# Kernel tuning notes

Hardware: AMD Instinct MI355X
Metric: run time of the kernel (lower is better)

Reference implementation:

```python
import jax, jax.numpy as jnp
import numpy as np

N_EMBED = 512  # codebook size per Quantize
EPS = 1e-8


def _quantize(x, embed):
    # x: (L, d) flattened tokens; embed: (d, K) codebook
    # squared euclidean distance via expansion (as in torch source)
    dist = (x * x).sum(1, keepdims=True) - 2.0 * (x @ embed) + (embed * embed).sum(0, keepdims=True)
    ind = jnp.argmin(dist, axis=1)                      # (L,)
    q = jnp.take(embed.T, ind, axis=0)                  # (L, d) embedding lookup
    diff = jnp.mean((jax.lax.stop_gradient(q) - x) ** 2)
    q_st = x + jax.lax.stop_gradient(q - x)             # straight-through
    return q_st, diff, ind


def _ot_score(x, embed):
    # x: (L, d); embed: (d, K). OT score = sum_k (1 - cos_sim) * softmax(x@embed / K)
    xn = x / (jnp.linalg.norm(x, axis=1, keepdims=True) + EPS)
    en = embed / (jnp.linalg.norm(embed, axis=0, keepdims=True) + EPS)
    cos_dissim = jax.lax.stop_gradient(1.0 - xn @ en)   # torch version uses .data (no grad)
    cnd = jax.nn.softmax((x @ embed) * (1.0 / embed.shape[1]), axis=1)
    return (cos_dissim * cnd).sum(1)                    # (L,)


def setup_inputs() -> dict:
    key = jax.random.key(0)
    k1, k2, k3, k4 = jax.random.split(key, 4)
    n_levels, B, L, d = 5, 128, 196, 64
    input_list = jax.random.normal(k1, (n_levels, B, L, d), dtype=jnp.float32)
    cb_top = jax.random.normal(k2, (15, d, N_EMBED), dtype=jnp.float32)        # quantize_list_5
    cb_lvl = jax.random.normal(k3, (4, 15, 2 * d, N_EMBED), dtype=jnp.float32)  # quantize_list_1..4
    label = jax.random.randint(k4, (B,), 0, 15, dtype=jnp.int32)
    return {"input_list": input_list, "cb_top": cb_top, "cb_lvl": cb_lvl, "label": label}


def reference(input_list, cb_top, cb_lvl, label):
    # Hierarchical switch-VQ encode (eval mode): top level quantized with per-class
    # codebook, then each lower level concatenated with top quantized code and
    # quantized with its own per-class codebook; last level also computes OT score.
    vq = jax.vmap(_quantize)
    emb_top = cb_top[label]                              # (B, 64, 512) per-sample codebook
    q4, d4, _ = vq(input_list[4], emb_top)               # (B, L, 64)
    diff = d4.sum()
    quants, ids = [], []
    ot_score = None
    for j in (3, 2, 1, 0):                               # quantize_list_4, _3, _2, _1
        x = jnp.concatenate([input_list[j], q4], axis=-1)  # (B, L, 128)
        emb = cb_lvl[j][label]                           # (B, 128, 512)
        q, d, i = vq(x, emb)
        diff = diff + d.sum()
        quants.append(q)
        ids.append(i)
        if j == 0:                                       # OT=True level
            ot_score = jax.vmap(_ot_score)(x, emb)       # (B, L)
    quant_list = jnp.stack(quants)                       # (4, B, L, 128)
    id_list = jnp.stack(ids)                             # (4, B, L)
    return quant_list, diff, id_list, ot_score
```

## Files before the change

### kernel.cpp

```cpp
#include <hip/hip_runtime.h>
#include <hip/hip_bf16.h>
#include <math.h>

#define B 128
#define L 196
#define K 512
#define NCLS 15
#define NT 32
#define NTILES 7

#define DIFF_OFF 12845056
#define ID_OFF   12845057
#define OT_OFF   12945409

#define WS_Q4   0
#define WS_N2   1605632
#define WS_INVE 1644032
#define WS_CBT  1651712
#define CBT_LVL 491520
#define WS_EBT_BYTES ((size_t)(1651712 + 4423680) * 4)
#define EBT_LVL_BYTES 983040

#define BAND 2.5f
#define CCAP 384

typedef __attribute__((ext_vector_type(8))) short s16x8;
typedef __attribute__((ext_vector_type(4))) float f32x4;
typedef __attribute__((ext_vector_type(4))) unsigned short u16x4;

__device__ inline unsigned short f2bf(float f) {
    __hip_bfloat16 h = __float2bfloat16(f);
    return *reinterpret_cast<unsigned short*>(&h);
}

__global__ __launch_bounds__(256) void precompute(
    const float* __restrict__ cb_top, const float* __restrict__ cb_lvl,
    float* __restrict__ ws)
{
    __shared__ float Ld[128][65];
    __shared__ float ps[64][4];
    const int m = blockIdx.x >> 3;
    const int c0 = (blockIdx.x & 7) * 64;
    const bool top = m < NCLS;
    const int D = top ? 64 : 128;
    const float* src = top ? cb_top + (size_t)m * 64 * K
                           : cb_lvl + (size_t)(m - NCLS) * 128 * K;
    float* cbT = ws + WS_CBT + (top ? (size_t)m * K * 64
                                    : (size_t)CBT_LVL + (size_t)(m - NCLS) * K * 128);
    unsigned short* ebt = (unsigned short*)((char*)ws + WS_EBT_BYTES +
        (top ? (size_t)m * K * 64 * 2
             : (size_t)EBT_LVL_BYTES + (size_t)(m - NCLS) * K * 128 * 2));
    const int tid = threadIdx.x;

    for (int e = tid; e < D * 64; e += 256) {
        int d = e >> 6, cc = e & 63;
        Ld[d][cc] = src[(size_t)d * K + c0 + cc];
    }
    __syncthreads();

    const int col = tid >> 2, q = tid & 3;
    const int seg = D >> 2;
    float ss = 0.f;
    for (int i = 0; i < seg; ++i) {
        int d = q * seg + i;
        float v = Ld[d][col];
        ss = fmaf(v, v, ss);
        cbT[(size_t)(c0 + col) * D + d] = v;
        ebt[(size_t)(c0 + col) * D + d] = f2bf(v);
    }
    ps[col][q] = ss;
    __syncthreads();
    if (tid < 64) {
        float n2 = (ps[tid][0] + ps[tid][1]) + (ps[tid][2] + ps[tid][3]);
        ws[WS_N2 + (size_t)m * K + c0 + tid] = n2;
        if (m >= NCLS && m < 2 * NCLS)
            ws[WS_INVE + (size_t)(m - NCLS) * K + c0 + tid] = 1.f / (sqrtf(n2) + 1e-8f);
    }
}

template<int D, bool IS_TOP, bool OT>
__global__ __launch_bounds__(256, 4) void vq_fused(
    const float* __restrict__ input, const int* __restrict__ label,
    float* __restrict__ ws, float* __restrict__ out, int jbase)
{
    constexpr int XS = D + 8;
    constexpr int NKS = D / 32;
    __shared__ unsigned short x_s[NT * XS];
    __shared__ float n2s[K];
    __shared__ float ivec[K];
    __shared__ float xn_s[NT];
    __shared__ float wmin_s[4][NT];
    __shared__ float rowMinG[NT];
    __shared__ unsigned int clist[CCAP];
    __shared__ float clv[CCAP];
    __shared__ int ccnt;
    __shared__ unsigned long long best_s[NT];
    __shared__ float otZ[4][NT], otW[4][NT];
    __shared__ float dred[4];

    const int tid = threadIdx.x;
    const int t0 = blockIdx.x * NT;
    const int b = blockIdx.y;
    const int j = IS_TOP ? 4 : (OT ? 0 : (int)blockIdx.z + jbase);
    const int c = label[b];

    const float* xin = input + ((size_t)((IS_TOP ? 4 : j) * B + b) * L) * 64;
    const float* q4w = ws + WS_Q4 + (size_t)b * L * 64;
    const float* n2w = ws + WS_N2 + (size_t)(IS_TOP ? c : NCLS + j * NCLS + c) * K;
    const char*  ebt = (const char*)ws + WS_EBT_BYTES +
        (IS_TOP ? (size_t)c * K * 64 * 2
                : (size_t)EBT_LVL_BYTES + (size_t)(j * NCLS + c) * K * 128 * 2);
    const float* cbT = ws + WS_CBT +
        (IS_TOP ? (size_t)c * K * 64
                : (size_t)CBT_LVL + (size_t)(j * NCLS + c) * K * 128);

    if (tid < NT) { xn_s[tid] = 0.f; best_s[tid] = ~0ULL; }
    if (tid == 0) ccnt = 0;
    for (int i = tid; i < K; i += 256) {
        n2s[i] = n2w[i];
        if (OT) ivec[i] = ws[WS_INVE + (size_t)c * K + i];
    }
    __syncthreads();

    for (int idx = tid; idx < NT * D / 4; idx += 256) {
        int row = idx / (D / 4);
        int k4 = (idx % (D / 4)) * 4;
        int l = t0 + row;
        float4 v = make_float4(0.f, 0.f, 0.f, 0.f);
        if (l < L) {
            const float* p = (IS_TOP || k4 < 64) ? xin + (size_t)l * 64 + k4
                                                 : q4w + (size_t)l * 64 + (k4 - 64);
            v = *reinterpret_cast<const float4*>(p);
            atomicAdd(&xn_s[row], v.x * v.x + v.y * v.y + v.z * v.z + v.w * v.w);
        }
        u16x4 h;
        h[0] = f2bf(v.x); h[1] = f2bf(v.y); h[2] = f2bf(v.z); h[3] = f2bf(v.w);
        *reinterpret_cast<u16x4*>(&x_s[row * XS + k4]) = h;
    }
    __syncthreads();

    const int wid = tid >> 6, lane = tid & 63;
    const int l15 = lane & 15, l4 = lane >> 4;

    float runMin[2][4];
    float zS[2][4], wS[2][4];
    #pragma unroll
    for (int mi = 0; mi < 2; ++mi)
        #pragma unroll
        for (int r = 0; r < 4; ++r) {
            runMin[mi][r] = 3.4e38f;
            if (OT) { zS[mi][r] = 0.f; wS[mi][r] = 0.f; }
        }

    for (int cc = 0; cc < 2; ++cc) {
        const int colbase = cc * 256 + wid * 64;
        f32x4 acc[2][4] = {};
        #pragma unroll
        for (int ks = 0; ks < NKS; ++ks) {
            s16x8 av[2], bv[4];
            #pragma unroll
            for (int mi = 0; mi < 2; ++mi)
                av[mi] = *reinterpret_cast<const s16x8*>(
                    &x_s[(mi * 16 + l15) * XS + ks * 32 + l4 * 8]);
            #pragma unroll
            for (int ni = 0; ni < 4; ++ni)
                bv[ni] = *reinterpret_cast<const s16x8*>(
                    ebt + ((size_t)(colbase + ni * 16 + l15) * D + ks * 32 + l4 * 8) * 2);
            #pragma unroll
            for (int mi = 0; mi < 2; ++mi)
                #pragma unroll
                for (int ni = 0; ni < 4; ++ni)
                    acc[mi][ni] = __builtin_amdgcn_mfma_f32_16x16x32_bf16(
                        av[mi], bv[ni], acc[mi][ni], 0, 0, 0);
        }
        #pragma unroll
        for (int mi = 0; mi < 2; ++mi) {
            #pragma unroll
            for (int r = 0; r < 4; ++r) {
                const int row = mi * 16 + l4 * 4 + r;
                const int lg = t0 + row;
                float dv[4];
                #pragma unroll
                for (int ni = 0; ni < 4; ++ni)
                    dv[ni] = n2s[colbase + ni * 16 + l15] - 2.f * acc[mi][ni][r];
                float mnW = fminf(fminf(dv[0], dv[1]), fminf(dv[2], dv[3]));
                #pragma unroll
                for (int s = 1; s <= 8; s <<= 1)
                    mnW = fminf(mnW, __shfl_xor(mnW, s, 64));
                runMin[mi][r] = fminf(runMin[mi][r], mnW);
                const float thr = runMin[mi][r] + BAND;
                if (lg < L) {
                    #pragma unroll
                    for (int ni = 0; ni < 4; ++ni) {
                        if (dv[ni] <= thr) {
                            int pos = atomicAdd(&ccnt, 1);
                            if (pos < CCAP) {
                                clist[pos] = ((unsigned)row << 16) |
                                             (unsigned)(colbase + ni * 16 + l15);
                                clv[pos] = dv[ni];
                            }
                        }
                    }
                }
                if (OT) {
                    float ivx = 1.f / (sqrtf(xn_s[row]) + 1e-8f);
                    #pragma unroll
                    for (int ni = 0; ni < 4; ++ni) {
                        float s = acc[mi][ni][r];
                        float e = __expf(s * (1.f / 512.f));
                        zS[mi][r] += e;
                        wS[mi][r] += (1.f - s * ivx * ivec[colbase + ni * 16 + l15]) * e;
                    }
                }
            }
        }
    }

    #pragma unroll
    for (int mi = 0; mi < 2; ++mi)
        #pragma unroll
        for (int r = 0; r < 4; ++r) {
            const int row = mi * 16 + l4 * 4 + r;
            if (l15 == 0) wmin_s[wid][row] = runMin[mi][r];
            if (OT) {
                float z = zS[mi][r], w = wS[mi][r];
                #pragma unroll
                for (int s = 1; s <= 8; s <<= 1) {
                    z += __shfl_xor(z, s, 64);
                    w += __shfl_xor(w, s, 64);
                }
                if (l15 == 0) { otZ[wid][row] = z; otW[wid][row] = w; }
            }
        }
    __syncthreads();
    if (tid < NT)
        rowMinG[tid] = fminf(fminf(wmin_s[0][tid], wmin_s[1][tid]),
                             fminf(wmin_s[2][tid], wmin_s[3][tid]));
    __syncthreads();

    {
        const int ncand = min(ccnt, CCAP);
        for (int e = wid; e < ncand; e += 4) {
            unsigned ent = clist[e];
            int row = ent >> 16, col = ent & 0xFFFF;
            if (clv[e] > rowMinG[row] + BAND) continue;
            int l = t0 + row;
            float prod;
            if (IS_TOP) {
                prod = xin[(size_t)l * 64 + lane] * cbT[(size_t)col * 64 + lane];
            } else {
                int k = lane * 2;
                const float* xp = (k < 64) ? &xin[(size_t)l * 64 + k]
                                           : &q4w[(size_t)l * 64 + (k - 64)];
                float2 xv = *reinterpret_cast<const float2*>(xp);
                float2 ev = *reinterpret_cast<const float2*>(&cbT[(size_t)col * 128 + k]);
                prod = xv.x * ev.x + xv.y * ev.y;
            }
            #pragma unroll
            for (int s = 1; s <= 32; s <<= 1) prod += __shfl_xor(prod, s, 64);
            if (lane == 0) {
                float dvE = n2s[col] - 2.f * prod;
                unsigned u = __float_as_uint(dvE);
                u = (u & 0x80000000u) ? ~u : (u | 0x80000000u);
                atomicMin(&best_s[row], ((unsigned long long)u << 32) | (unsigned)col);
            }
        }
    }
    __syncthreads();

    float dacc = 0.f;
    const int slot = IS_TOP ? 0 : 3 - j;
    for (int rr = wid; rr < NT; rr += 4) {
        int l = t0 + rr;
        if (l >= L) continue;
        unsigned long long key = best_s[rr];
        unsigned col = (unsigned)(key & 0xFFFFFFFFull);
        unsigned u = (unsigned)(key >> 32);
        u = (u & 0x80000000u) ? (u & 0x7FFFFFFFu) : ~u;
        float dvE = __uint_as_float(u);
        if (lane == 0) dacc += dvE + xn_s[rr];
        if (IS_TOP) {
            ws[WS_Q4 + ((size_t)b * L + l) * 64 + lane] = cbT[(size_t)col * 64 + lane];
        } else {
            int k = lane * 2;
            float2 ev = *reinterpret_cast<const float2*>(&cbT[(size_t)col * 128 + k]);
            *reinterpret_cast<float2*>(
                &out[(((size_t)slot * B + b) * L + l) * 128 + k]) = ev;
            if (lane == 0) {
                out[ID_OFF + ((size_t)slot * B + b) * L + l] = (float)col;
                if (OT) {
                    float z = (otZ[0][rr] + otZ[1][rr]) + (otZ[2][rr] + otZ[3][rr]);
                    float w = (otW[0][rr] + otW[1][rr]) + (otW[2][rr] + otW[3][rr]);
                    out[OT_OFF + (size_t)b * L + l] = w / z;
                }
            }
        }
    }
    if (lane == 0) dred[wid] = dacc;
    __syncthreads();
    if (tid == 0)
        atomicAdd(out + DIFF_OFF,
                  ((dred[0] + dred[1]) + (dred[2] + dred[3])) * (1.f / (L * (float)D)));
}

extern "C" void kernel_launch(void* const* d_in, const int* in_sizes, int n_in,
                              void* d_out, int out_size, void* d_ws, size_t ws_size,
                              hipStream_t stream) {
    const float* input  = (const float*)d_in[0];
    const float* cb_top = (const float*)d_in[1];
    const float* cb_lvl = (const float*)d_in[2];
    const int*   label  = (const int*)d_in[3];
    float* out = (float*)d_out;
    float* ws  = (float*)d_ws;

    hipMemsetAsync(out + DIFF_OFF, 0, sizeof(float), stream);

    precompute<<<600, 256, 0, stream>>>(cb_top, cb_lvl, ws);
    vq_fused<64, true, false><<<dim3(NTILES, B, 1), 256, 0, stream>>>(input, label, ws, out, 0);
    vq_fused<128, false, false><<<dim3(NTILES, B, 3), 256, 0, stream>>>(input, label, ws, out, 1);
    vq_fused<128, false, true><<<dim3(NTILES, B, 1), 256, 0, stream>>>(input, label, ws, out, 0);
}
```

Measured before the change: 327.0 us.

## Fuse top-level and lower-level VQ into one kernel, recomputing top per block

Replaces the three VQ launches (top level, then three lower levels, then the OT level) with one kernel over four levels. Each block recomputes the top-level quantization for its tile in shared memory instead of reading q4 from a global workspace written by a separate launch. This removes the launch serialization and the q4 round trip through global memory, at the cost of doing the top-level GEMM and refine four times. It also re-maps the refine and output phases to 16-lane groups with float4 loads, keeps n2 and inverse norms in registers, raises the candidate cap, and asks for occupancy 6.

```diff
diff --git a/kernel.cpp b/kernel.cpp
--- a/kernel.cpp
+++ b/kernel.cpp
@@ -13,16 +13,15 @@
 #define ID_OFF   12845057
 #define OT_OFF   12945409
 
-#define WS_Q4   0
-#define WS_N2   1605632
-#define WS_INVE 1644032
-#define WS_CBT  1651712
+#define WS_N2   0
+#define WS_INVE 38400
+#define WS_CBT  46080
 #define CBT_LVL 491520
-#define WS_EBT_BYTES ((size_t)(1651712 + 4423680) * 4)
+#define WS_EBT_BYTES ((size_t)(46080 + 4469760) * 4)
 #define EBT_LVL_BYTES 983040
 
 #define BAND 2.5f
-#define CCAP 384
+#define CCAP 512
 
 typedef __attribute__((ext_vector_type(8))) short s16x8;
 typedef __attribute__((ext_vector_type(4))) float f32x4;
@@ -78,94 +77,89 @@
     }
 }
 
-template<int D, bool IS_TOP, bool OT>
-__global__ __launch_bounds__(256, 4) void vq_fused(
+__global__ __launch_bounds__(256, 6) void vq_all(
     const float* __restrict__ input, const int* __restrict__ label,
-    float* __restrict__ ws, float* __restrict__ out, int jbase)
+    float* __restrict__ ws, float* __restrict__ out)
 {
-    constexpr int XS = D + 8;
-    constexpr int NKS = D / 32;
-    __shared__ unsigned short x_s[NT * XS];
-    __shared__ float n2s[K];
-    __shared__ float ivec[K];
-    __shared__ float xn_s[NT];
+    __shared__ char uA[8192];
+    __shared__ unsigned short xL_s[NT * 136];
+    __shared__ float clv[CCAP];
+    __shared__ unsigned int clist[CCAP];
     __shared__ float wmin_s[4][NT];
     __shared__ float rowMinG[NT];
-    __shared__ unsigned int clist[CCAP];
-    __shared__ float clv[CCAP];
+    __shared__ unsigned long long best_s[NT];
+    __shared__ float xn4_s[NT], xnL_s[NT], xnq_s[NT];
+    __shared__ float otZ_s[NT], otW_s[NT];
+    __shared__ float dacc_s;
     __shared__ int ccnt;
-    __shared__ unsigned long long best_s[NT];
-    __shared__ float otZ[4][NT], otW[4][NT];
-    __shared__ float dred[4];
+
+    unsigned short* x4_s = (unsigned short*)uA;
+    float* q4f = (float*)uA;
 
     const int tid = threadIdx.x;
     const int t0 = blockIdx.x * NT;
     const int b = blockIdx.y;
-    const int j = IS_TOP ? 4 : (OT ? 0 : (int)blockIdx.z + jbase);
+    const int j = blockIdx.z;
+    const bool OT = (j == 0);
+    const bool addTop = (j == 3);
     const int c = label[b];
 
-    const float* xin = input + ((size_t)((IS_TOP ? 4 : j) * B + b) * L) * 64;
-    const float* q4w = ws + WS_Q4 + (size_t)b * L * 64;
-    const float* n2w = ws + WS_N2 + (size_t)(IS_TOP ? c : NCLS + j * NCLS + c) * K;
-    const char*  ebt = (const char*)ws + WS_EBT_BYTES +
-        (IS_TOP ? (size_t)c * K * 64 * 2
-                : (size_t)EBT_LVL_BYTES + (size_t)(j * NCLS + c) * K * 128 * 2);
-    const float* cbT = ws + WS_CBT +
-        (IS_TOP ? (size_t)c * K * 64
-                : (size_t)CBT_LVL + (size_t)(j * NCLS + c) * K * 128);
-
-    if (tid < NT) { xn_s[tid] = 0.f; best_s[tid] = ~0ULL; }
-    if (tid == 0) ccnt = 0;
-    for (int i = tid; i < K; i += 256) {
-        n2s[i] = n2w[i];
-        if (OT) ivec[i] = ws[WS_INVE + (size_t)c * K + i];
-    }
-    __syncthreads();
-
-    for (int idx = tid; idx < NT * D / 4; idx += 256) {
-        int row = idx / (D / 4);
-        int k4 = (idx % (D / 4)) * 4;
+    const float* xin4 = input + ((size_t)(4 * B + b) * L) * 64;
+    const float* xinj = input + ((size_t)(j * B + b) * L) * 64;
+    const float* n2T = ws + WS_N2 + (size_t)c * K;
+    const float* n2L = ws + WS_N2 + (size_t)(NCLS + j * NCLS + c) * K;
+    const float* ive = ws + WS_INVE + (size_t)c * K;
+    const float* cbT_T = ws + WS_CBT + (size_t)c * (K * 64);
+    const float* cbT_L = ws + WS_CBT + CBT_LVL + (size_t)(j * NCLS + c) * (K * 128);
+    const unsigned short* ebT =
+        (const unsigned short*)((const char*)ws + WS_EBT_BYTES) + (size_t)c * (K * 64);
+    const unsigned short* ebL =
+        (const unsigned short*)((const char*)ws + WS_EBT_BYTES + EBT_LVL_BYTES) +
+        (size_t)(j * NCLS + c) * (K * 128);
+
+    const int wid = tid >> 6, lane = tid & 63, l15 = lane & 15, l4 = lane >> 4;
+
+    if (tid < NT) {
+        xn4_s[tid] = 0.f; xnL_s[tid] = 0.f; best_s[tid] = ~0ULL;
+        otZ_s[tid] = 0.f; otW_s[tid] = 0.f;
+    }
+    if (tid == 0) { ccnt = 0; dacc_s = 0.f; }
+    __syncthreads();
+
+    for (int idx = tid; idx < NT * 16; idx += 256) {
+        int row = idx >> 4, k4 = (idx & 15) << 2;
         int l = t0 + row;
         float4 v = make_float4(0.f, 0.f, 0.f, 0.f);
         if (l < L) {
-            const float* p = (IS_TOP || k4 < 64) ? xin + (size_t)l * 64 + k4
-                                                 : q4w + (size_t)l * 64 + (k4 - 64);
-            v = *reinterpret_cast<const float4*>(p);
-            atomicAdd(&xn_s[row], v.x * v.x + v.y * v.y + v.z * v.z + v.w * v.w);
-        }
-        u16x4 h;
-        h[0] = f2bf(v.x); h[1] = f2bf(v.y); h[2] = f2bf(v.z); h[3] = f2bf(v.w);
-        *reinterpret_cast<u16x4*>(&x_s[row * XS + k4]) = h;
-    }
-    __syncthreads();
-
-    const int wid = tid >> 6, lane = tid & 63;
-    const int l15 = lane & 15, l4 = lane >> 4;
+            v = *(const float4*)(xin4 + (size_t)l * 64 + k4);
+            atomicAdd(&xn4_s[row], v.x * v.x + v.y * v.y + v.z * v.z + v.w * v.w);
+        }
+        u16x4 h; h[0] = f2bf(v.x); h[1] = f2bf(v.y); h[2] = f2bf(v.z); h[3] = f2bf(v.w);
+        *(u16x4*)&x4_s[row * 72 + k4] = h;
+    }
+    __syncthreads();
 
     float runMin[2][4];
-    float zS[2][4], wS[2][4];
     #pragma unroll
     for (int mi = 0; mi < 2; ++mi)
         #pragma unroll
-        for (int r = 0; r < 4; ++r) {
-            runMin[mi][r] = 3.4e38f;
-            if (OT) { zS[mi][r] = 0.f; wS[mi][r] = 0.f; }
-        }
+        for (int r = 0; r < 4; ++r) runMin[mi][r] = 3.4e38f;
 
     for (int cc = 0; cc < 2; ++cc) {
         const int colbase = cc * 256 + wid * 64;
+        float n2v[4];
+        #pragma unroll
+        for (int ni = 0; ni < 4; ++ni) n2v[ni] = n2T[colbase + ni * 16 + l15];
         f32x4 acc[2][4] = {};
         #pragma unroll
-        for (int ks = 0; ks < NKS; ++ks) {
+        for (int ks = 0; ks < 2; ++ks) {
             s16x8 av[2], bv[4];
             #pragma unroll
             for (int mi = 0; mi < 2; ++mi)
-                av[mi] = *reinterpret_cast<const s16x8*>(
-                    &x_s[(mi * 16 + l15) * XS + ks * 32 + l4 * 8]);
+                av[mi] = *(const s16x8*)&x4_s[(mi * 16 + l15) * 72 + ks * 32 + l4 * 8];
             #pragma unroll
             for (int ni = 0; ni < 4; ++ni)
-                bv[ni] = *reinterpret_cast<const s16x8*>(
-                    ebt + ((size_t)(colbase + ni * 16 + l15) * D + ks * 32 + l4 * 8) * 2);
+                bv[ni] = *(const s16x8*)&ebT[(size_t)(colbase + ni * 16 + l15) * 64 + ks * 32 + l4 * 8];
             #pragma unroll
             for (int mi = 0; mi < 2; ++mi)
                 #pragma unroll
@@ -178,18 +172,156 @@
             #pragma unroll
             for (int r = 0; r < 4; ++r) {
                 const int row = mi * 16 + l4 * 4 + r;
-                const int lg = t0 + row;
                 float dv[4];
                 #pragma unroll
                 for (int ni = 0; ni < 4; ++ni)
-                    dv[ni] = n2s[colbase + ni * 16 + l15] - 2.f * acc[mi][ni][r];
+                    dv[ni] = n2v[ni] - 2.f * acc[mi][ni][r];
                 float mnW = fminf(fminf(dv[0], dv[1]), fminf(dv[2], dv[3]));
                 #pragma unroll
                 for (int s = 1; s <= 8; s <<= 1)
                     mnW = fminf(mnW, __shfl_xor(mnW, s, 64));
                 runMin[mi][r] = fminf(runMin[mi][r], mnW);
                 const float thr = runMin[mi][r] + BAND;
-                if (lg < L) {
+                if (t0 + row < L) {
+                    #pragma unroll
+                    for (int ni = 0; ni < 4; ++ni) {
+                        if (dv[ni] <= thr) {
+                            int pos = atomicAdd(&ccnt, 1);
+                            if (pos < CCAP) {
+                                clist[pos] = ((unsigned)row << 16) |
+                                             (unsigned)(colbase + ni * 16 + l15);
+                                clv[pos] = dv[ni];
+                            }
+                        }
+                    }
+                }
+            }
+        }
+    }
+    #pragma unroll
+    for (int mi = 0; mi < 2; ++mi)
+        #pragma unroll
+        for (int r = 0; r < 4; ++r)
+            if (l15 == 0) wmin_s[wid][mi * 16 + l4 * 4 + r] = runMin[mi][r];
+    __syncthreads();
+    if (tid < NT)
+        rowMinG[tid] = fminf(fminf(wmin_s[0][tid], wmin_s[1][tid]),
+                             fminf(wmin_s[2][tid], wmin_s[3][tid]));
+    __syncthreads();
+
+    {
+        const int ncand = min(ccnt, CCAP);
+        const int g = tid >> 4, li = tid & 15;
+        for (int e = g; e < ncand; e += 16) {
+            unsigned ent = clist[e];
+            int row = ent >> 16, col = ent & 0xFFFF;
+            if (clv[e] > rowMinG[row] + BAND) continue;
+            int l = t0 + row;
+            float4 xv = *(const float4*)(xin4 + (size_t)l * 64 + li * 4);
+            float4 ev = *(const float4*)(cbT_T + (size_t)col * 64 + li * 4);
+            float prod = xv.x * ev.x + xv.y * ev.y + xv.z * ev.z + xv.w * ev.w;
+            #pragma unroll
+            for (int s = 1; s <= 8; s <<= 1) prod += __shfl_xor(prod, s, 64);
+            if (li == 0) {
+                float dvE = n2T[col] - 2.f * prod;
+                unsigned u = __float_as_uint(dvE);
+                u = (u & 0x80000000u) ? ~u : (u | 0x80000000u);
+                atomicMin(&best_s[row], ((unsigned long long)u << 32) | (unsigned)col);
+            }
+        }
+    }
+    __syncthreads();
+
+    {
+        const int g = tid >> 4, li = tid & 15;
+        for (int rr = g; rr < NT; rr += 16) {
+            int l = t0 + rr;
+            unsigned long long key = best_s[rr];
+            float4 ev = make_float4(0.f, 0.f, 0.f, 0.f);
+            float dvE = 0.f;
+            if (l < L) {
+                unsigned col = (unsigned)(key & 0xFFFFFFFFull);
+                unsigned u = (unsigned)(key >> 32);
+                u = (u & 0x80000000u) ? (u & 0x7FFFFFFFu) : ~u;
+                dvE = __uint_as_float(u);
+                ev = *(const float4*)(cbT_T + (size_t)col * 64 + li * 4);
+            }
+            *(float4*)&q4f[rr * 64 + li * 4] = ev;
+            u16x4 h; h[0] = f2bf(ev.x); h[1] = f2bf(ev.y); h[2] = f2bf(ev.z); h[3] = f2bf(ev.w);
+            *(u16x4*)&xL_s[rr * 136 + 64 + li * 4] = h;
+            float qs = ev.x * ev.x + ev.y * ev.y + ev.z * ev.z + ev.w * ev.w;
+            #pragma unroll
+            for (int s = 1; s <= 8; s <<= 1) qs += __shfl_xor(qs, s, 64);
+            if (li == 0) {
+                xnq_s[rr] = qs;
+                if (addTop && l < L)
+                    atomicAdd(&dacc_s, (dvE + xn4_s[rr]) * (1.f / (L * 64.f)));
+            }
+        }
+    }
+    __syncthreads();
+
+    if (tid < NT) best_s[tid] = ~0ULL;
+    if (tid == 0) ccnt = 0;
+    for (int idx = tid; idx < NT * 16; idx += 256) {
+        int row = idx >> 4, k4 = (idx & 15) << 2;
+        int l = t0 + row;
+        float4 v = make_float4(0.f, 0.f, 0.f, 0.f);
+        if (l < L) {
+            v = *(const float4*)(xinj + (size_t)l * 64 + k4);
+            atomicAdd(&xnL_s[row], v.x * v.x + v.y * v.y + v.z * v.z + v.w * v.w);
+        }
+        u16x4 h; h[0] = f2bf(v.x); h[1] = f2bf(v.y); h[2] = f2bf(v.z); h[3] = f2bf(v.w);
+        *(u16x4*)&xL_s[row * 136 + k4] = h;
+    }
+    __syncthreads();
+
+    #pragma unroll
+    for (int mi = 0; mi < 2; ++mi)
+        #pragma unroll
+        for (int r = 0; r < 4; ++r) runMin[mi][r] = 3.4e38f;
+
+    for (int cc = 0; cc < 2; ++cc) {
+        const int colbase = cc * 256 + wid * 64;
+        float n2v[4], iv[4];
+        #pragma unroll
+        for (int ni = 0; ni < 4; ++ni) {
+            n2v[ni] = n2L[colbase + ni * 16 + l15];
+            if (OT) iv[ni] = ive[colbase + ni * 16 + l15];
+        }
+        f32x4 acc[2][4] = {};
+        #pragma unroll
+        for (int ks = 0; ks < 4; ++ks) {
+            s16x8 av[2], bv[4];
+            #pragma unroll
+            for (int mi = 0; mi < 2; ++mi)
+                av[mi] = *(const s16x8*)&xL_s[(mi * 16 + l15) * 136 + ks * 32 + l4 * 8];
+            #pragma unroll
+            for (int ni = 0; ni < 4; ++ni)
+                bv[ni] = *(const s16x8*)&ebL[(size_t)(colbase + ni * 16 + l15) * 128 + ks * 32 + l4 * 8];
+            #pragma unroll
+            for (int mi = 0; mi < 2; ++mi)
+                #pragma unroll
+                for (int ni = 0; ni < 4; ++ni)
+                    acc[mi][ni] = __builtin_amdgcn_mfma_f32_16x16x32_bf16(
+                        av[mi], bv[ni], acc[mi][ni], 0, 0, 0);
+        }
+        #pragma unroll
+        for (int mi = 0; mi < 2; ++mi) {
+            #pragma unroll
+            for (int r = 0; r < 4; ++r) {
+                const int row = mi * 16 + l4 * 4 + r;
+                float dv[4];
+                #pragma unroll
+                for (int ni = 0; ni < 4; ++ni)
+                    dv[ni] = n2v[ni] - 2.f * acc[mi][ni][r];
+                float mnW = fminf(fminf(dv[0], dv[1]), fminf(dv[2], dv[3]));
+                #pragma unroll
+                for (int s = 1; s <= 8; s <<= 1)
+                    mnW = fminf(mnW, __shfl_xor(mnW, s, 64));
+                runMin[mi][r] = fminf(runMin[mi][r], mnW);
+                const float thr = runMin[mi][r] + BAND;
+                if (t0 + row < L) {
                     #pragma unroll
                     for (int ni = 0; ni < 4; ++ni) {
                         if (dv[ni] <= thr) {
@@ -203,35 +335,34 @@
                     }
                 }
                 if (OT) {
-                    float ivx = 1.f / (sqrtf(xn_s[row]) + 1e-8f);
+                    float xn = xnL_s[row] + xnq_s[row];
+                    float ivx = 1.f / (sqrtf(xn) + 1e-8f);
+                    float zloc = 0.f, wloc = 0.f;
                     #pragma unroll
                     for (int ni = 0; ni < 4; ++ni) {
                         float s = acc[mi][ni][r];
                         float e = __expf(s * (1.f / 512.f));
-                        zS[mi][r] += e;
-                        wS[mi][r] += (1.f - s * ivx * ivec[colbase + ni * 16 + l15]) * e;
+                        zloc += e;
+                        wloc += (1.f - s * ivx * iv[ni]) * e;
+                    }
+                    #pragma unroll
+                    for (int s = 1; s <= 8; s <<= 1) {
+                        zloc += __shfl_xor(zloc, s, 64);
+                        wloc += __shfl_xor(wloc, s, 64);
+                    }
+                    if (l15 == 0) {
+                        atomicAdd(&otZ_s[row], zloc);
+                        atomicAdd(&otW_s[row], wloc);
                     }
                 }
             }
         }
     }
-
     #pragma unroll
     for (int mi = 0; mi < 2; ++mi)
         #pragma unroll
-        for (int r = 0; r < 4; ++r) {
-            const int row = mi * 16 + l4 * 4 + r;
-            if (l15 == 0) wmin_s[wid][row] = runMin[mi][r];
-            if (OT) {
-                float z = zS[mi][r], w = wS[mi][r];
-                #pragma unroll
-                for (int s = 1; s <= 8; s <<= 1) {
-                    z += __shfl_xor(z, s, 64);
-                    w += __shfl_xor(w, s, 64);
-                }
-                if (l15 == 0) { otZ[wid][row] = z; otW[wid][row] = w; }
-            }
-        }
+        for (int r = 0; r < 4; ++r)
+            if (l15 == 0) wmin_s[wid][mi * 16 + l4 * 4 + r] = runMin[mi][r];
     __syncthreads();
     if (tid < NT)
         rowMinG[tid] = fminf(fminf(wmin_s[0][tid], wmin_s[1][tid]),
@@ -240,26 +371,29 @@
 
     {
         const int ncand = min(ccnt, CCAP);
-        for (int e = wid; e < ncand; e += 4) {
+        const int g = tid >> 4, li = tid & 15;
+        for (int e = g; e < ncand; e += 16) {
             unsigned ent = clist[e];
             int row = ent >> 16, col = ent & 0xFFFF;
             if (clv[e] > rowMinG[row] + BAND) continue;
             int l = t0 + row;
-            float prod;
-            if (IS_TOP) {
-                prod = xin[(size_t)l * 64 + lane] * cbT[(size_t)col * 64 + lane];
+            int k = li * 8;
+            float4 xa, xb;
+            if (li < 8) {
+                xa = *(const float4*)(xinj + (size_t)l * 64 + k);
+                xb = *(const float4*)(xinj + (size_t)l * 64 + k + 4);
             } else {
-                int k = lane * 2;
-                const float* xp = (k < 64) ? &xin[(size_t)l * 64 + k]
-                                           : &q4w[(size_t)l * 64 + (k - 64)];
-                float2 xv = *reinterpret_cast<const float2*>(xp);
-                float2 ev = *reinterpret_cast<const float2*>(&cbT[(size_t)col * 128 + k]);
-                prod = xv.x * ev.x + xv.y * ev.y;
-            }
-            #pragma unroll
-            for (int s = 1; s <= 32; s <<= 1) prod += __shfl_xor(prod, s, 64);
-            if (lane == 0) {
-                float dvE = n2s[col] - 2.f * prod;
+                xa = *(const float4*)&q4f[row * 64 + (k - 64)];
+                xb = *(const float4*)&q4f[row * 64 + (k - 60)];
+            }
+            float4 ea = *(const float4*)(cbT_L + (size_t)col * 128 + k);
+            float4 eb = *(const float4*)(cbT_L + (size_t)col * 128 + k + 4);
+            float prod = xa.x * ea.x + xa.y * ea.y + xa.z * ea.z + xa.w * ea.w +
+                         xb.x * eb.x + xb.y * eb.y + xb.z * eb.z + xb.w * eb.w;
+            #pragma unroll
+            for (int s = 1; s <= 8; s <<= 1) prod += __shfl_xor(prod, s, 64);
+            if (li == 0) {
+                float dvE = n2L[col] - 2.f * prod;
                 unsigned u = __float_as_uint(dvE);
                 u = (u & 0x80000000u) ? ~u : (u | 0x80000000u);
                 atomicMin(&best_s[row], ((unsigned long long)u << 32) | (unsigned)col);
@@ -268,39 +402,31 @@
     }
     __syncthreads();
 
-    float dacc = 0.f;
-    const int slot = IS_TOP ? 0 : 3 - j;
-    for (int rr = wid; rr < NT; rr += 4) {
-        int l = t0 + rr;
-        if (l >= L) continue;
-        unsigned long long key = best_s[rr];
-        unsigned col = (unsigned)(key & 0xFFFFFFFFull);
-        unsigned u = (unsigned)(key >> 32);
-        u = (u & 0x80000000u) ? (u & 0x7FFFFFFFu) : ~u;
-        float dvE = __uint_as_float(u);
-        if (lane == 0) dacc += dvE + xn_s[rr];
-        if (IS_TOP) {
-            ws[WS_Q4 + ((size_t)b * L + l) * 64 + lane] = cbT[(size_t)col * 64 + lane];
-        } else {
-            int k = lane * 2;
-            float2 ev = *reinterpret_cast<const float2*>(&cbT[(size_t)col * 128 + k]);
-            *reinterpret_cast<float2*>(
-                &out[(((size_t)slot * B + b) * L + l) * 128 + k]) = ev;
-            if (lane == 0) {
+    {
+        const int slot = 3 - j;
+        const int g = tid >> 4, li = tid & 15;
+        for (int rr = g; rr < NT; rr += 16) {
+            int l = t0 + rr;
+            if (l >= L) continue;
+            unsigned long long key = best_s[rr];
+            unsigned col = (unsigned)(key & 0xFFFFFFFFull);
+            unsigned u = (unsigned)(key >> 32);
+            u = (u & 0x80000000u) ? (u & 0x7FFFFFFFu) : ~u;
+            float dvE = __uint_as_float(u);
+            float4 ea = *(const float4*)(cbT_L + (size_t)col * 128 + li * 8);
+            float4 eb = *(const float4*)(cbT_L + (size_t)col * 128 + li * 8 + 4);
+            float* dst = out + (((size_t)slot * B + b) * L + l) * 128 + li * 8;
+            *(float4*)dst = ea;
+            *(float4*)(dst + 4) = eb;
+            if (li == 0) {
                 out[ID_OFF + ((size_t)slot * B + b) * L + l] = (float)col;
-                if (OT) {
-                    float z = (otZ[0][rr] + otZ[1][rr]) + (otZ[2][rr] + otZ[3][rr]);
-                    float w = (otW[0][rr] + otW[1][rr]) + (otW[2][rr] + otW[3][rr]);
-                    out[OT_OFF + (size_t)b * L + l] = w / z;
-                }
-            }
-        }
-    }
-    if (lane == 0) dred[wid] = dacc;
-    __syncthreads();
-    if (tid == 0)
-        atomicAdd(out + DIFF_OFF,
-                  ((dred[0] + dred[1]) + (dred[2] + dred[3])) * (1.f / (L * (float)D)));
+                if (OT) out[OT_OFF + (size_t)b * L + l] = otW_s[rr] / otZ_s[rr];
+                atomicAdd(&dacc_s, (dvE + xnL_s[rr] + xnq_s[rr]) * (1.f / (L * 128.f)));
+            }
+        }
+    }
+    __syncthreads();
+    if (tid == 0) atomicAdd(out + DIFF_OFF, dacc_s);
 }
 
 extern "C" void kernel_launch(void* const* d_in, const int* in_sizes, int n_in,
@@ -316,7 +442,5 @@
     hipMemsetAsync(out + DIFF_OFF, 0, sizeof(float), stream);
 
     precompute<<<600, 256, 0, stream>>>(cb_top, cb_lvl, ws);
-    vq_fused<64, true, false><<<dim3(NTILES, B, 1), 256, 0, stream>>>(input, label, ws, out, 0);
-    vq_fused<128, false, false><<<dim3(NTILES, B, 3), 256, 0, stream>>>(input, label, ws, out, 1);
-    vq_fused<128, false, true><<<dim3(NTILES, B, 1), 256, 0, stream>>>(input, label, ws, out, 0);
+    vq_all<<<dim3(NTILES, B, 4), 256, 0, stream>>>(input, label, ws, out);
 }
```

After: 346.1 us. 1.06x slower.
